# Optimization experiments

Hardware: AMD Instinct MI355X
Metric: run time of the kernel (lower is better)

## Reference

```python
import jax, jax.numpy as jnp
import numpy as np

B, N, D_IN, D_OUT, H = 2, 2048, 1024, 1024, 16
HD = D_OUT // H


def setup_inputs() -> dict:
    key = jax.random.key(0)
    ks = jax.random.split(key, 6)
    s_in = 1.0 / np.sqrt(D_IN)
    s_out = 1.0 / np.sqrt(D_OUT)
    return {
        "x": jax.random.normal(ks[0], (B, N, D_IN), dtype=jnp.float32),
        "Wq": jax.random.uniform(ks[1], (D_IN, D_OUT), jnp.float32, -s_in, s_in),
        "Wk": jax.random.uniform(ks[2], (D_IN, D_OUT), jnp.float32, -s_in, s_in),
        "Wv": jax.random.uniform(ks[3], (D_IN, D_OUT), jnp.float32, -s_in, s_in),
        "Wo": jax.random.uniform(ks[4], (D_OUT, D_OUT), jnp.float32, -s_out, s_out),
        "bo": jax.random.uniform(ks[5], (D_OUT,), jnp.float32, -s_out, s_out),
    }


def reference(x, Wq, Wk, Wv, Wo, bo):
    b, n, _ = x.shape
    # project and split heads: [b, n, d_out] -> [b, h, n, hd]
    def heads(w):
        return w.reshape(b, n, H, HD).transpose(0, 2, 1, 3)
    q = heads(x @ Wq)
    k = heads(x @ Wk)
    v = heads(x @ Wv)
    # materialized causal attention (dropout rate 0.0 -> identity)
    scores = jnp.einsum("bhqd,bhkd->bhqk", q, k)
    causal = jnp.tril(jnp.ones((n, n), dtype=bool))  # keep lower triangle
    scores = jnp.where(causal, scores, -jnp.inf)
    attn = jax.nn.softmax(scores / np.sqrt(HD), axis=-1)
    ctx = jnp.einsum("bhqk,bhkd->bhqd", attn, v)
    ctx = ctx.transpose(0, 2, 1, 3).reshape(b, n, D_OUT)
    return ctx @ Wo + bo
```

## Files before the change

### kernel.cpp

```cpp
#include <hip/hip_runtime.h>
#include <math.h>
#include <stdint.h>

#define B_ 2
#define N_ 2048
#define D_ 1024
#define H_ 16
#define HD_ 64
#define M_ (B_ * N_)

typedef __bf16 bf16x8 __attribute__((ext_vector_type(8)));
typedef float f32x4 __attribute__((ext_vector_type(4)));

__device__ __forceinline__ ushort bfbits(float f) {
    __bf16 h = (__bf16)f;
    return __builtin_bit_cast(ushort, h);
}

__device__ __forceinline__ void glds16(const ushort* g, ushort* l) {
    __builtin_amdgcn_global_load_lds(
        (const __attribute__((address_space(1))) uint32_t*)g,
        (__attribute__((address_space(3))) uint32_t*)l, 16, 0, 0);
}

__global__ __launch_bounds__(256) void cvt_x(const float* __restrict__ x,
                                             ushort* __restrict__ xb) {
    int i = blockIdx.x * 256 + threadIdx.x;
    float4 v = ((const float4*)x)[i];
    ushort4 o;
    o.x = bfbits(v.x); o.y = bfbits(v.y); o.z = bfbits(v.z); o.w = bfbits(v.w);
    ((ushort4*)xb)[i] = o;
}

__global__ __launch_bounds__(256) void cvt_w(const float* __restrict__ W0,
                                             const float* __restrict__ W1,
                                             const float* __restrict__ W2,
                                             const float* __restrict__ W3,
                                             ushort* __restrict__ Wt) {
    __shared__ float T[32][33];
    const float* W = (blockIdx.z == 0) ? W0 : (blockIdx.z == 1) ? W1
                   : (blockIdx.z == 2) ? W2 : W3;
    ushort* out = Wt + (size_t)blockIdx.z * D_ * D_;
    const int t = threadIdx.x;
    const int k0 = blockIdx.x * 32, n0 = blockIdx.y * 32;
    {
        int kl = t >> 3, nl = (t & 7) * 4;
        float4 v = *(const float4*)&W[(size_t)(k0 + kl) * D_ + n0 + nl];
        T[kl][nl] = v.x; T[kl][nl + 1] = v.y; T[kl][nl + 2] = v.z; T[kl][nl + 3] = v.w;
    }
    __syncthreads();
    {
        int nl = t >> 3, k4 = (t & 7) * 4;
        ushort4 o;
        o.x = bfbits(T[k4 + 0][nl]); o.y = bfbits(T[k4 + 1][nl]);
        o.z = bfbits(T[k4 + 2][nl]); o.w = bfbits(T[k4 + 3][nl]);
        *(ushort4*)&out[(size_t)(n0 + nl) * D_ + k0 + k4] = o;
    }
}

__global__ __launch_bounds__(256) void transp_v(const ushort* __restrict__ vb,
                                                ushort* __restrict__ vt) {
    __shared__ ushort T[64][72];
    const int t = threadIdx.x;
    const int nt = blockIdx.x, bh = blockIdx.y;
    const ushort* src = vb + ((size_t)bh * N_ + nt * 64) * HD_;
    #pragma unroll
    for (int it = 0; it < 2; ++it) {
        int fi = it * 256 + t;
        int r = fi >> 3, c = (fi & 7) * 8;
        *(uint4*)&T[r][c] = *(const uint4*)&src[(size_t)r * HD_ + c];
    }
    __syncthreads();
    ushort* dst = vt + (size_t)bh * HD_ * N_ + nt * 64;
    #pragma unroll
    for (int it = 0; it < 2; ++it) {
        int fi = it * 256 + t;
        int hd = fi >> 3, n0 = (fi & 7) * 8;
        uint4 o;
        o.x = (uint32_t)T[n0 + 0][hd] | ((uint32_t)T[n0 + 1][hd] << 16);
        o.y = (uint32_t)T[n0 + 2][hd] | ((uint32_t)T[n0 + 3][hd] << 16);
        o.z = (uint32_t)T[n0 + 4][hd] | ((uint32_t)T[n0 + 5][hd] << 16);
        o.w = (uint32_t)T[n0 + 6][hd] | ((uint32_t)T[n0 + 7][hd] << 16);
        *(uint4*)&dst[(size_t)hd * N_ + n0] = o;
    }
}

#define BK 32

__device__ __forceinline__ void gemm_tile(const ushort* __restrict__ A,
                                          const ushort* __restrict__ Bt,
                                          int K, int tileM, int tileN,
                                          ushort* As, ushort* Bs,
                                          f32x4 acc[4][4]) {
    const int t = threadIdx.x;
    const int l = t & 63;
    const int w = __builtin_amdgcn_readfirstlane(t >> 6);
    const int wr = w >> 1, wc = w & 1;
    const int li = l & 15, lg = l >> 4;
    const int lr = l >> 2;
    const int colu = (((l & 3) ^ (lr & 3)) << 3);
    const int swz = (li & 3) << 3;

    for (int k0 = 0; k0 < K; k0 += BK) {
        __syncthreads();
        #pragma unroll
        for (int it = 0; it < 2; ++it) {
            const int c2 = it * 4 + w;
            const int row = c2 * 16 + lr;
            glds16(&A[(size_t)(tileM + row) * K + k0 + colu], &As[c2 * 512]);
            glds16(&Bt[(size_t)(tileN + row) * K + k0 + colu], &Bs[c2 * 512]);
        }
        __syncthreads();
        bf16x8 a[4], b[4];
        #pragma unroll
        for (int m = 0; m < 4; ++m)
            a[m] = *(const bf16x8*)&As[(wr * 64 + m * 16 + li) * 32 + ((lg << 3) ^ swz)];
        #pragma unroll
        for (int n = 0; n < 4; ++n)
            b[n] = *(const bf16x8*)&Bs[(wc * 64 + n * 16 + li) * 32 + ((lg << 3) ^ swz)];
        #pragma unroll
        for (int m = 0; m < 4; ++m)
            #pragma unroll
            for (int n = 0; n < 4; ++n)
                acc[m][n] = __builtin_amdgcn_mfma_f32_16x16x32_bf16(a[m], b[n], acc[m][n], 0, 0, 0);
    }
}

#define QSCALE 0.180336880f

__global__ __launch_bounds__(256) void qkv_gemm(const ushort* __restrict__ xb,
                                                const ushort* __restrict__ Wt,
                                                ushort* __restrict__ q,
                                                ushort* __restrict__ k,
                                                ushort* __restrict__ v) {
    __shared__ ushort As[128 * 32];
    __shared__ ushort Bs[128 * 32];
    f32x4 acc[4][4];
    #pragma unroll
    for (int m = 0; m < 4; ++m)
        #pragma unroll
        for (int n = 0; n < 4; ++n)
            acc[m][n] = (f32x4){0.f, 0.f, 0.f, 0.f};

    const int tileM = blockIdx.x * 128;
    const int wsel = blockIdx.y >> 3;
    const int tileN = (blockIdx.y & 7) * 128;
    const ushort* Bmat = Wt + (size_t)wsel * D_ * D_;

    gemm_tile(xb, Bmat, D_, tileM, tileN, As, Bs, acc);

    ushort* out = (wsel == 0) ? q : (wsel == 1) ? k : v;
    const float scale = (wsel == 0) ? QSCALE : 1.0f;
    const int l = threadIdx.x & 63, w = threadIdx.x >> 6;
    const int wr = w >> 1, wc = w & 1;
    const int li = l & 15, lg = l >> 4;
    #pragma unroll
    for (int m = 0; m < 4; ++m)
        #pragma unroll
        for (int n = 0; n < 4; ++n)
            #pragma unroll
            for (int r = 0; r < 4; ++r) {
                int grow = tileM + wr * 64 + m * 16 + lg * 4 + r;
                int gcol = tileN + wc * 64 + n * 16 + li;
                int b = grow >> 11, nn = grow & (N_ - 1);
                int h = gcol >> 6, hd = gcol & 63;
                out[((size_t)(b * H_ + h) * N_ + nn) * HD_ + hd] = bfbits(acc[m][n][r] * scale);
            }
}

__global__ __launch_bounds__(256) void out_gemm(const ushort* __restrict__ ctx,
                                                const ushort* __restrict__ Wt,
                                                const float* __restrict__ bo,
                                                float* __restrict__ outp) {
    __shared__ ushort As[128 * 32];
    __shared__ ushort Bs[128 * 32];
    f32x4 acc[4][4];
    #pragma unroll
    for (int m = 0; m < 4; ++m)
        #pragma unroll
        for (int n = 0; n < 4; ++n)
            acc[m][n] = (f32x4){0.f, 0.f, 0.f, 0.f};

    const int tileM = blockIdx.x * 128;
    const int tileN = blockIdx.y * 128;
    const ushort* Bmat = Wt + (size_t)3 * D_ * D_;

    gemm_tile(ctx, Bmat, D_, tileM, tileN, As, Bs, acc);

    const int l = threadIdx.x & 63, w = threadIdx.x >> 6;
    const int wr = w >> 1, wc = w & 1;
    const int li = l & 15, lg = l >> 4;
    #pragma unroll
    for (int n = 0; n < 4; ++n) {
        float bias = bo[tileN + wc * 64 + n * 16 + li];
        #pragma unroll
        for (int m = 0; m < 4; ++m)
            #pragma unroll
            for (int r = 0; r < 4; ++r) {
                int grow = tileM + wr * 64 + m * 16 + lg * 4 + r;
                int gcol = tileN + wc * 64 + n * 16 + li;
                outp[(size_t)grow * D_ + gcol] = acc[m][n][r] + bias;
            }
    }
}

__global__ __launch_bounds__(256) void attn_fwd(const ushort* __restrict__ q,
                                                const ushort* __restrict__ k,
                                                const ushort* __restrict__ vt,
                                                ushort* __restrict__ ctx) {
    __shared__ ushort Ks[2][64 * 64];
    __shared__ ushort Vs[2][64 * 64];
    __shared__ ushort Ps[4][16][72];

    const int t = threadIdx.x;
    const int l = t & 63;
    const int w = __builtin_amdgcn_readfirstlane(t >> 6);
    const int li = l & 15, lg = l >> 4;
    const int f = blockIdx.x;
    const int bh = ((f & 7) << 2) | ((f >> 3) & 3);
    const int pj = f >> 5;

    const ushort* Qg = q + (size_t)bh * N_ * HD_;
    const ushort* Kg = k + (size_t)bh * N_ * HD_;
    const ushort* Vg = vt + (size_t)bh * HD_ * N_;
    const int b = bh >> 4, h = bh & 15;

    const int r8 = l >> 3;
    const int soff = ((l & 7) ^ r8) * 8;
    const int rswz = li & 7;

    for (int task = 0; task < 2; ++task) {
        const int qt = (task == 0) ? pj : 31 - pj;
        const int nkb = qt + 1;
        const int qb64 = qt * 64 + w * 16;
        const int qg = qb64 + li;

        bf16x8 bq[2];
        #pragma unroll
        for (int tk = 0; tk < 2; ++tk)
            bq[tk] = *(const bf16x8*)&Qg[(size_t)qg * HD_ + tk * 32 + lg * 8];

        f32x4 od[4];
        #pragma unroll
        for (int db = 0; db < 4; ++db) od[db] = (f32x4){0.f, 0.f, 0.f, 0.f};
        float mrun = -INFINITY, lsum = 0.f;

        #pragma unroll
        for (int i = 0; i < 2; ++i) {
            const int seg = w + i * 4;
            const int row = seg * 8 + r8;
            glds16(&Kg[(size_t)row * HD_ + soff], &Ks[0][seg * 512]);
            glds16(&Vg[(size_t)row * N_ + soff], &Vs[0][seg * 512]);
        }
        __syncthreads();

        int cur = 0;
        for (int kb = 0; kb < nkb; ++kb) {
            if (kb + 1 < nkb) {
                #pragma unroll
                for (int i = 0; i < 2; ++i) {
                    const int seg = w + i * 4;
                    const int row = seg * 8 + r8;
                    glds16(&Kg[(size_t)((kb + 1) * 64 + row) * HD_ + soff], &Ks[cur ^ 1][seg * 512]);
                    glds16(&Vg[(size_t)row * N_ + (kb + 1) * 64 + soff], &Vs[cur ^ 1][seg * 512]);
                }
            }

            f32x4 st[4];
            #pragma unroll
            for (int c = 0; c < 4; ++c) {
                st[c] = (f32x4){0.f, 0.f, 0.f, 0.f};
                #pragma unroll
                for (int tk = 0; tk < 2; ++tk) {
                    bf16x8 kf = *(const bf16x8*)&Ks[cur][(c * 16 + li) * 64 + (((tk * 4 + lg) ^ rswz) * 8)];
                    st[c] = __builtin_amdgcn_mfma_f32_16x16x32_bf16(kf, bq[tk], st[c], 0, 0, 0);
                }
            }

            const bool lastkb = (kb == qt);
            float sv[4][4];
            #pragma unroll
            for (int c = 0; c < 4; ++c)
                #pragma unroll
                for (int r = 0; r < 4; ++r) {
                    const int kgl = kb * 64 + c * 16 + lg * 4 + r;
                    sv[c][r] = (lastkb && kgl > qg) ? -INFINITY : st[c][r];
                }

            float mx = fmaxf(fmaxf(sv[0][0], sv[0][1]), fmaxf(sv[0][2], sv[0][3]));
            #pragma unroll
            for (int c = 1; c < 4; ++c)
                mx = fmaxf(mx, fmaxf(fmaxf(sv[c][0], sv[c][1]), fmaxf(sv[c][2], sv[c][3])));
            mx = fmaxf(mx, __shfl_xor(mx, 16));
            mx = fmaxf(mx, __shfl_xor(mx, 32));

            if (!__all(mx - mrun <= 8.f)) {
                const float mn = fmaxf(mrun, mx);
                const float al = exp2f(mrun - mn);
                lsum *= al;
                mrun = mn;
                float ar[4];
                #pragma unroll
                for (int r = 0; r < 4; ++r) ar[r] = __shfl(al, lg * 4 + r);
                #pragma unroll
                for (int db = 0; db < 4; ++db)
                    #pragma unroll
                    for (int r = 0; r < 4; ++r) od[db][r] *= ar[r];
            }

            float rs = 0.f;
            #pragma unroll
            for (int c = 0; c < 4; ++c) {
                float p0 = exp2f(sv[c][0] - mrun);
                float p1 = exp2f(sv[c][1] - mrun);
                float p2 = exp2f(sv[c][2] - mrun);
                float p3 = exp2f(sv[c][3] - mrun);
                rs += (p0 + p1) + (p2 + p3);
                uint2 pk;
                pk.x = (uint32_t)bfbits(p0) | ((uint32_t)bfbits(p1) << 16);
                pk.y = (uint32_t)bfbits(p2) | ((uint32_t)bfbits(p3) << 16);
                *(uint2*)&Ps[w][li][c * 16 + lg * 4] = pk;
            }
            rs += __shfl_xor(rs, 16);
            rs += __shfl_xor(rs, 32);
            lsum += rs;

            #pragma unroll
            for (int tj = 0; tj < 2; ++tj) {
                bf16x8 pa = *(const bf16x8*)&Ps[w][li][tj * 32 + lg * 8];
                #pragma unroll
                for (int db = 0; db < 4; ++db) {
                    bf16x8 bv = *(const bf16x8*)&Vs[cur][(db * 16 + li) * 64 + (((tj * 4 + lg) ^ rswz) * 8)];
                    od[db] = __builtin_amdgcn_mfma_f32_16x16x32_bf16(pa, bv, od[db], 0, 0, 0);
                }
            }

            __syncthreads();
            cur ^= 1;
        }

        #pragma unroll
        for (int r = 0; r < 4; ++r) {
            const float inv = 1.f / __shfl(lsum, lg * 4 + r);
            const int grow = qb64 + lg * 4 + r;
            #pragma unroll
            for (int db = 0; db < 4; ++db)
                ctx[((size_t)(b * N_ + grow)) * D_ + h * 64 + db * 16 + li] = bfbits(od[db][r] * inv);
        }
    }
}

extern "C" void kernel_launch(void* const* d_in, const int* in_sizes, int n_in,
                              void* d_out, int out_size, void* d_ws, size_t ws_size,
                              hipStream_t stream) {
    (void)in_sizes; (void)n_in; (void)out_size; (void)ws_size;
    const float* x  = (const float*)d_in[0];
    const float* Wq = (const float*)d_in[1];
    const float* Wk = (const float*)d_in[2];
    const float* Wv = (const float*)d_in[3];
    const float* Wo = (const float*)d_in[4];
    const float* bo = (const float*)d_in[5];
    float* outp = (float*)d_out;

    ushort* xb  = (ushort*)d_ws;
    ushort* Wt  = xb + (size_t)M_ * D_;
    ushort* qb  = Wt + (size_t)4 * D_ * D_;
    ushort* kb  = qb + (size_t)B_ * H_ * N_ * HD_;
    ushort* vb  = kb + (size_t)B_ * H_ * N_ * HD_;
    ushort* vtb = vb + (size_t)B_ * H_ * N_ * HD_;
    ushort* ctx = vtb + (size_t)B_ * H_ * N_ * HD_;

    cvt_x<<<dim3((M_ * D_ / 4) / 256), 256, 0, stream>>>(x, xb);
    cvt_w<<<dim3(32, 32, 4), 256, 0, stream>>>(Wq, Wk, Wv, Wo, Wt);
    qkv_gemm<<<dim3(32, 24), 256, 0, stream>>>(xb, Wt, qb, kb, vb);
    transp_v<<<dim3(32, 32), 256, 0, stream>>>(vb, vtb);
    attn_fwd<<<dim3(512), 256, 0, stream>>>(qb, kb, vtb, ctx);
    out_gemm<<<dim3(32, 8), 256, 0, stream>>>(ctx, Wt, bo, outp);
}
```

Measured before the change: 124.2 us.

## Launch one q-tile per block and peel masked diagonal step from causal loop

The attention kernel no longer pairs a short and long query tile per block. It launches 1024 blocks, each handling one query tile, ordered longest-first so heavy blocks are scheduled early. The causal-mask select is moved out of the main loop into a separate final diagonal step, and the prefetch branch is removed. This trades the paired-tile load balancing for more parallelism and relies on hardware scheduling to balance the uneven block lengths.

```diff
diff --git a/kernel.cpp b/kernel.cpp
--- a/kernel.cpp
+++ b/kernel.cpp
@@ -204,6 +204,77 @@
     }
 }
 
+#define ATTN_STEP(CUR, KB, MASKED)                                             \
+{                                                                              \
+    const ushort* Kb_ = Ks[CUR];                                               \
+    const ushort* Vb_ = Vs[CUR];                                               \
+    f32x4 st[4];                                                               \
+    _Pragma("unroll")                                                          \
+    for (int c = 0; c < 4; ++c) {                                              \
+        st[c] = (f32x4){0.f, 0.f, 0.f, 0.f};                                   \
+        _Pragma("unroll")                                                      \
+        for (int tk = 0; tk < 2; ++tk) {                                       \
+            bf16x8 kf = *(const bf16x8*)&Kb_[(c * 16 + li) * 64 +              \
+                                             (((tk * 4 + lg) ^ rswz) * 8)];    \
+            st[c] = __builtin_amdgcn_mfma_f32_16x16x32_bf16(kf, bq[tk], st[c], 0, 0, 0); \
+        }                                                                      \
+    }                                                                          \
+    if (MASKED) {                                                              \
+        _Pragma("unroll")                                                      \
+        for (int c = 0; c < 4; ++c)                                            \
+            _Pragma("unroll")                                                  \
+            for (int r = 0; r < 4; ++r) {                                      \
+                const int kgl = (KB) * 64 + c * 16 + lg * 4 + r;               \
+                if (kgl > qg) st[c][r] = -INFINITY;                            \
+            }                                                                  \
+    }                                                                          \
+    float mx = fmaxf(fmaxf(st[0][0], st[0][1]), fmaxf(st[0][2], st[0][3]));    \
+    _Pragma("unroll")                                                          \
+    for (int c = 1; c < 4; ++c)                                                \
+        mx = fmaxf(mx, fmaxf(fmaxf(st[c][0], st[c][1]), fmaxf(st[c][2], st[c][3]))); \
+    mx = fmaxf(mx, __shfl_xor(mx, 16));                                        \
+    mx = fmaxf(mx, __shfl_xor(mx, 32));                                        \
+    if (!__all(mx - mrun <= 8.f)) {                                            \
+        const float mn = fmaxf(mrun, mx);                                      \
+        const float al = exp2f(mrun - mn);                                     \
+        lsum *= al;                                                            \
+        mrun = mn;                                                             \
+        float ar[4];                                                           \
+        _Pragma("unroll")                                                      \
+        for (int r = 0; r < 4; ++r) ar[r] = __shfl(al, lg * 4 + r);            \
+        _Pragma("unroll")                                                      \
+        for (int db = 0; db < 4; ++db)                                         \
+            _Pragma("unroll")                                                  \
+            for (int r = 0; r < 4; ++r) od[db][r] *= ar[r];                    \
+    }                                                                          \
+    float rs = 0.f;                                                            \
+    _Pragma("unroll")                                                          \
+    for (int c = 0; c < 4; ++c) {                                              \
+        float p0 = exp2f(st[c][0] - mrun);                                     \
+        float p1 = exp2f(st[c][1] - mrun);                                     \
+        float p2 = exp2f(st[c][2] - mrun);                                     \
+        float p3 = exp2f(st[c][3] - mrun);                                     \
+        rs += (p0 + p1) + (p2 + p3);                                           \
+        uint2 pk;                                                              \
+        pk.x = (uint32_t)bfbits(p0) | ((uint32_t)bfbits(p1) << 16);            \
+        pk.y = (uint32_t)bfbits(p2) | ((uint32_t)bfbits(p3) << 16);            \
+        *(uint2*)&Ps[w][li][c * 16 + lg * 4] = pk;                             \
+    }                                                                          \
+    rs += __shfl_xor(rs, 16);                                                  \
+    rs += __shfl_xor(rs, 32);                                                  \
+    lsum += rs;                                                                \
+    _Pragma("unroll")                                                          \
+    for (int tj = 0; tj < 2; ++tj) {                                           \
+        bf16x8 pa = *(const bf16x8*)&Ps[w][li][tj * 32 + lg * 8];              \
+        _Pragma("unroll")                                                      \
+        for (int db = 0; db < 4; ++db) {                                       \
+            bf16x8 bv = *(const bf16x8*)&Vb_[(db * 16 + li) * 64 +             \
+                                             (((tj * 4 + lg) ^ rswz) * 8)];    \
+            od[db] = __builtin_amdgcn_mfma_f32_16x16x32_bf16(pa, bv, od[db], 0, 0, 0); \
+        }                                                                      \
+    }                                                                          \
+}
+
 __global__ __launch_bounds__(256) void attn_fwd(const ushort* __restrict__ q,
                                                 const ushort* __restrict__ k,
                                                 const ushort* __restrict__ vt,
@@ -218,7 +289,7 @@
     const int li = l & 15, lg = l >> 4;
     const int f = blockIdx.x;
     const int bh = ((f & 7) << 2) | ((f >> 3) & 3);
-    const int pj = f >> 5;
+    const int qt = 31 - (f >> 5);
 
     const ushort* Qg = q + (size_t)bh * N_ * HD_;
     const ushort* Kg = k + (size_t)bh * N_ * HD_;
@@ -229,124 +300,50 @@
     const int soff = ((l & 7) ^ r8) * 8;
     const int rswz = li & 7;
 
-    for (int task = 0; task < 2; ++task) {
-        const int qt = (task == 0) ? pj : 31 - pj;
-        const int nkb = qt + 1;
-        const int qb64 = qt * 64 + w * 16;
-        const int qg = qb64 + li;
-
-        bf16x8 bq[2];
-        #pragma unroll
-        for (int tk = 0; tk < 2; ++tk)
-            bq[tk] = *(const bf16x8*)&Qg[(size_t)qg * HD_ + tk * 32 + lg * 8];
-
-        f32x4 od[4];
-        #pragma unroll
-        for (int db = 0; db < 4; ++db) od[db] = (f32x4){0.f, 0.f, 0.f, 0.f};
-        float mrun = -INFINITY, lsum = 0.f;
-
+    const int qb64 = qt * 64 + w * 16;
+    const int qg = qb64 + li;
+
+    bf16x8 bq[2];
+    #pragma unroll
+    for (int tk = 0; tk < 2; ++tk)
+        bq[tk] = *(const bf16x8*)&Qg[(size_t)qg * HD_ + tk * 32 + lg * 8];
+
+    f32x4 od[4];
+    #pragma unroll
+    for (int db = 0; db < 4; ++db) od[db] = (f32x4){0.f, 0.f, 0.f, 0.f};
+    float mrun = -INFINITY, lsum = 0.f;
+
+    #pragma unroll
+    for (int i = 0; i < 2; ++i) {
+        const int seg = w + i * 4;
+        const int row = seg * 8 + r8;
+        glds16(&Kg[(size_t)row * HD_ + soff], &Ks[0][seg * 512]);
+        glds16(&Vg[(size_t)row * N_ + soff], &Vs[0][seg * 512]);
+    }
+    __syncthreads();
+
+    int cur = 0;
+    for (int kb = 0; kb < qt; ++kb) {
         #pragma unroll
         for (int i = 0; i < 2; ++i) {
             const int seg = w + i * 4;
             const int row = seg * 8 + r8;
-            glds16(&Kg[(size_t)row * HD_ + soff], &Ks[0][seg * 512]);
-            glds16(&Vg[(size_t)row * N_ + soff], &Vs[0][seg * 512]);
+            glds16(&Kg[(size_t)((kb + 1) * 64 + row) * HD_ + soff], &Ks[cur ^ 1][seg * 512]);
+            glds16(&Vg[(size_t)row * N_ + (kb + 1) * 64 + soff], &Vs[cur ^ 1][seg * 512]);
         }
+        ATTN_STEP(cur, kb, false)
         __syncthreads();
-
-        int cur = 0;
-        for (int kb = 0; kb < nkb; ++kb) {
-            if (kb + 1 < nkb) {
-                #pragma unroll
-                for (int i = 0; i < 2; ++i) {
-                    const int seg = w + i * 4;
-                    const int row = seg * 8 + r8;
-                    glds16(&Kg[(size_t)((kb + 1) * 64 + row) * HD_ + soff], &Ks[cur ^ 1][seg * 512]);
-                    glds16(&Vg[(size_t)row * N_ + (kb + 1) * 64 + soff], &Vs[cur ^ 1][seg * 512]);
-                }
-            }
-
-            f32x4 st[4];
-            #pragma unroll
-            for (int c = 0; c < 4; ++c) {
-                st[c] = (f32x4){0.f, 0.f, 0.f, 0.f};
-                #pragma unroll
-                for (int tk = 0; tk < 2; ++tk) {
-                    bf16x8 kf = *(const bf16x8*)&Ks[cur][(c * 16 + li) * 64 + (((tk * 4 + lg) ^ rswz) * 8)];
-                    st[c] = __builtin_amdgcn_mfma_f32_16x16x32_bf16(kf, bq[tk], st[c], 0, 0, 0);
-                }
-            }
-
-            const bool lastkb = (kb == qt);
-            float sv[4][4];
-            #pragma unroll
-            for (int c = 0; c < 4; ++c)
-                #pragma unroll
-                for (int r = 0; r < 4; ++r) {
-                    const int kgl = kb * 64 + c * 16 + lg * 4 + r;
-                    sv[c][r] = (lastkb && kgl > qg) ? -INFINITY : st[c][r];
-                }
-
-            float mx = fmaxf(fmaxf(sv[0][0], sv[0][1]), fmaxf(sv[0][2], sv[0][3]));
-            #pragma unroll
-            for (int c = 1; c < 4; ++c)
-                mx = fmaxf(mx, fmaxf(fmaxf(sv[c][0], sv[c][1]), fmaxf(sv[c][2], sv[c][3])));
-            mx = fmaxf(mx, __shfl_xor(mx, 16));
-            mx = fmaxf(mx, __shfl_xor(mx, 32));
-
-            if (!__all(mx - mrun <= 8.f)) {
-                const float mn = fmaxf(mrun, mx);
-                const float al = exp2f(mrun - mn);
-                lsum *= al;
-                mrun = mn;
-                float ar[4];
-                #pragma unroll
-                for (int r = 0; r < 4; ++r) ar[r] = __shfl(al, lg * 4 + r);
-                #pragma unroll
-                for (int db = 0; db < 4; ++db)
-                    #pragma unroll
-                    for (int r = 0; r < 4; ++r) od[db][r] *= ar[r];
-            }
-
-            float rs = 0.f;
-            #pragma unroll
-            for (int c = 0; c < 4; ++c) {
-                float p0 = exp2f(sv[c][0] - mrun);
-                float p1 = exp2f(sv[c][1] - mrun);
-                float p2 = exp2f(sv[c][2] - mrun);
-                float p3 = exp2f(sv[c][3] - mrun);
-                rs += (p0 + p1) + (p2 + p3);
-                uint2 pk;
-                pk.x = (uint32_t)bfbits(p0) | ((uint32_t)bfbits(p1) << 16);
-                pk.y = (uint32_t)bfbits(p2) | ((uint32_t)bfbits(p3) << 16);
-                *(uint2*)&Ps[w][li][c * 16 + lg * 4] = pk;
-            }
-            rs += __shfl_xor(rs, 16);
-            rs += __shfl_xor(rs, 32);
-            lsum += rs;
-
-            #pragma unroll
-            for (int tj = 0; tj < 2; ++tj) {
-                bf16x8 pa = *(const bf16x8*)&Ps[w][li][tj * 32 + lg * 8];
-                #pragma unroll
-                for (int db = 0; db < 4; ++db) {
-                    bf16x8 bv = *(const bf16x8*)&Vs[cur][(db * 16 + li) * 64 + (((tj * 4 + lg) ^ rswz) * 8)];
-                    od[db] = __builtin_amdgcn_mfma_f32_16x16x32_bf16(pa, bv, od[db], 0, 0, 0);
-                }
-            }
-
-            __syncthreads();
-            cur ^= 1;
-        }
-
-        #pragma unroll
-        for (int r = 0; r < 4; ++r) {
-            const float inv = 1.f / __shfl(lsum, lg * 4 + r);
-            const int grow = qb64 + lg * 4 + r;
-            #pragma unroll
-            for (int db = 0; db < 4; ++db)
-                ctx[((size_t)(b * N_ + grow)) * D_ + h * 64 + db * 16 + li] = bfbits(od[db][r] * inv);
-        }
+        cur ^= 1;
+    }
+    ATTN_STEP(cur, qt, true)
+
+    #pragma unroll
+    for (int r = 0; r < 4; ++r) {
+        const float inv = 1.f / __shfl(lsum, lg * 4 + r);
+        const int grow = qb64 + lg * 4 + r;
+        #pragma unroll
+        for (int db = 0; db < 4; ++db)
+            ctx[((size_t)(b * N_ + grow)) * D_ + h * 64 + db * 16 + li] = bfbits(od[db][r] * inv);
     }
 }
 
@@ -374,6 +371,6 @@
     cvt_w<<<dim3(32, 32, 4), 256, 0, stream>>>(Wq, Wk, Wv, Wo, Wt);
     qkv_gemm<<<dim3(32, 24), 256, 0, stream>>>(xb, Wt, qb, kb, vb);
     transp_v<<<dim3(32, 32), 256, 0, stream>>>(vb, vtb);
-    attn_fwd<<<dim3(512), 256, 0, stream>>>(qb, kb, vtb, ctx);
+    attn_fwd<<<dim3(1024), 256, 0, stream>>>(qb, kb, vtb, ctx);
     out_gemm<<<dim3(32, 8), 256, 0, stream>>>(ctx, Wt, bo, outp);
 }
```

Result: faster. 119.2 us (-4.1%).
